# Kernel optimization log

Measured on AMD Instinct MI355X. Metric: run time of the kernel, lower is better.

Reference implementation:

```python
import jax, jax.numpy as jnp
import numpy as np

B, NPG, DEG = 16, 2048, 16          # graphs, nodes per graph, avg degree
N_TOT = B * NPG
E_TOT = N_TOT * DEG
NEG_SLOPE = 0.2


def _gat(x, src, dst, n, w, a_src, a_dst, b):
    # PyG GATConv: concat heads, add self loops, leaky_relu(0.2), segment softmax over targets
    H, C = a_src.shape
    h = (x @ w.T).reshape(n, H, C)                       # [n,H,C]
    sl = jnp.arange(n, dtype=src.dtype)
    s = jnp.concatenate([src, sl])
    d = jnp.concatenate([dst, sl])
    e = jax.nn.leaky_relu((h * a_src).sum(-1)[s] + (h * a_dst).sum(-1)[d], NEG_SLOPE)  # [E+n,H]
    emax = jax.lax.stop_gradient(jax.ops.segment_max(e, d, num_segments=n))
    ee = jnp.exp(e - emax[d])
    alpha = ee / (jax.ops.segment_sum(ee, d, num_segments=n)[d] + 1e-16)
    out = jax.ops.segment_sum(alpha[:, :, None] * h[s], d, num_segments=n)  # [n,H,C]
    return out.reshape(n, H * C) + b


def _gcn(x, src, dst, mask, n, w, b):
    # PyG GCNConv with self loops + symmetric norm; mask = float edge validity
    h = x @ w.T
    deg = jax.ops.segment_sum(mask, dst, num_segments=n) + 1.0  # +1 for self loop
    dinv = jax.lax.rsqrt(deg)
    coef = dinv[src] * dinv[dst] * mask
    out = jax.ops.segment_sum(coef[:, None] * h[src], dst, num_segments=n) + (dinv * dinv)[:, None] * h
    return out + b


def _sag(x, src, dst, mask, b_graphs, npg, k, w_rel, b_rel, w_root):
    # PyG SAGPooling(ratio=0.5): GraphConv score, per-graph top-k, x[perm]*tanh(score[perm]), filter_adj
    n = b_graphs * npg
    agg = jax.ops.segment_sum(mask[:, None] * x[src], dst, num_segments=n)
    score = (agg @ w_rel.T + b_rel + x @ w_root.T)[:, 0]      # [n]
    _, idx = jax.lax.top_k(score.reshape(b_graphs, npg), k)    # [B,k]
    perm = (jnp.arange(b_graphs, dtype=jnp.int32)[:, None] * npg + idx).reshape(-1)
    x_new = x[perm] * jnp.tanh(score[perm])[:, None]
    new_id = jnp.full((n,), -1, jnp.int32).at[perm].set(jnp.arange(b_graphs * k, dtype=jnp.int32))
    ns, nd = new_id[src], new_id[dst]
    valid = mask * ((ns >= 0) & (nd >= 0)).astype(x.dtype)
    return x_new, jnp.maximum(ns, 0), jnp.maximum(nd, 0), valid


def setup_inputs() -> dict:
    key = jax.random.key(0)
    ks = jax.random.split(key, 32)

    def lin(k, o, i):
        return (jax.random.normal(k, (o, i), jnp.float32) / np.sqrt(i)).astype(jnp.float32)

    x = jax.random.normal(ks[0], (N_TOT, 64), jnp.float32)
    off = jnp.repeat(jnp.arange(B, dtype=jnp.int32) * NPG, NPG * DEG)
    src = off + jax.random.randint(ks[1], (E_TOT,), 0, NPG, jnp.int32)
    dst = off + jax.random.randint(ks[2], (E_TOT,), 0, NPG, jnp.int32)
    edge_index = jnp.stack([src, dst])
    batch = jnp.repeat(jnp.arange(B, dtype=jnp.int32), NPG)

    return {
        'x': x, 'edge_index': edge_index, 'batch': batch,
        'gat1_w': lin(ks[3], 256, 64), 'gat1_asrc': lin(ks[4], 4, 64), 'gat1_adst': lin(ks[5], 4, 64),
        'gat1_b': jnp.zeros((256,), jnp.float32),
        'gat2_w': lin(ks[6], 256, 256), 'gat2_asrc': lin(ks[7], 4, 64), 'gat2_adst': lin(ks[8], 4, 64),
        'gat2_b': jnp.zeros((256,), jnp.float32),
        # pooling GCN1: 256 -> 128
        'gcn1_w': lin(ks[9], 128, 256), 'gcn1_b': jnp.zeros((128,), jnp.float32),
        'sag1_wrel': lin(ks[10], 1, 128), 'sag1_brel': jnp.zeros((1,), jnp.float32), 'sag1_wroot': lin(ks[11], 1, 128),
        # pooling GCN2: 128 -> 128
        'gcn2_w': lin(ks[12], 128, 128), 'gcn2_b': jnp.zeros((128,), jnp.float32),
        'sag2_wrel': lin(ks[13], 1, 128), 'sag2_brel': jnp.zeros((1,), jnp.float32), 'sag2_wroot': lin(ks[14], 1, 128),
        # classifier 128 -> 256 -> 128 -> 10
        'fc1_w': lin(ks[15], 256, 128), 'fc1_b': jnp.zeros((256,), jnp.float32),
        'fc2_w': lin(ks[16], 128, 256), 'fc2_b': jnp.zeros((128,), jnp.float32),
        'out_w': lin(ks[17], 10, 128), 'out_b': jnp.zeros((10,), jnp.float32),
    }


def reference(x, edge_index, batch,
              gat1_w, gat1_asrc, gat1_adst, gat1_b,
              gat2_w, gat2_asrc, gat2_adst, gat2_b,
              gcn1_w, gcn1_b, sag1_wrel, sag1_brel, sag1_wroot,
              gcn2_w, gcn2_b, sag2_wrel, sag2_brel, sag2_wroot,
              fc1_w, fc1_b, fc2_w, fc2_b, out_w, out_b):
    n = x.shape[0]
    src, dst = edge_index[0], edge_index[1]
    ones = jnp.ones(src.shape[0], x.dtype)

    # GAT encoder
    h = jax.nn.relu(_gat(x, src, dst, n, gat1_w, gat1_asrc, gat1_adst, gat1_b))
    h = _gat(h, src, dst, n, gat2_w, gat2_asrc, gat2_adst, gat2_b)  # [n,256]

    # GCN + SAGPool x2
    h = jax.nn.relu(_gcn(h, src, dst, ones, n, gcn1_w, gcn1_b))
    k1 = NPG // 2
    h, s1, d1, m1 = _sag(h, src, dst, ones, B, NPG, k1, sag1_wrel, sag1_brel, sag1_wroot)
    h = jax.nn.relu(_gcn(h, s1, d1, m1, B * k1, gcn2_w, gcn2_b))
    k2 = k1 // 2
    h, s2, d2, m2 = _sag(h, s1, d1, m1, B, k1, k2, sag2_wrel, sag2_brel, sag2_wroot)

    # global mean pool (equal-size graphs -> simple reshape-mean; batch vec implied)
    g = h.reshape(B, k2, -1).mean(axis=1)  # [B,128]

    # classifier MLP
    g = jax.nn.relu(g @ fc1_w.T + fc1_b)
    g = jax.nn.relu(g @ fc2_w.T + fc2_b)
    return g @ out_w.T + out_b  # [B,10]
```

## Files before the change

kernel.cpp:

```cpp
#include <hip/hip_runtime.h>

#define N1 32768
#define EE 524288
#define NB 16
#define DEG 16
#define NPG1 2048
#define KK1 1024
#define N2 16384
#define NPG2 1024
#define KK2 512
#define N3 8192

typedef _Float16 half8_t __attribute__((ext_vector_type(8)));
typedef float floatx16 __attribute__((ext_vector_type(16)));

static __device__ __forceinline__ float leaky(float x){ return fmaxf(x, 0.2f*x); }

__global__ void count_dst(const int* __restrict__ dst, int* __restrict__ cnt, int E){
    int i = blockIdx.x*blockDim.x + threadIdx.x;
    if (i < E) atomicAdd(&cnt[dst[i]], 1);
}

__global__ void remap_count(const int* __restrict__ src, const int* __restrict__ dst,
                            const int* __restrict__ nid, int* __restrict__ ns,
                            int* __restrict__ nd, int* __restrict__ cnt, int E){
    int i = blockIdx.x*blockDim.x + threadIdx.x;
    if (i < E){
        int a = nid[src[i]], b = nid[dst[i]];
        ns[i] = a; nd[i] = b;
        if (a >= 0 && b >= 0) atomicAdd(&cnt[b], 1);
    }
}

__global__ void blocksum_k(const int* __restrict__ cnt, int* __restrict__ bs){
    __shared__ int red[4];
    int tid = threadIdx.x;
    int v = cnt[blockIdx.x*256 + tid];
    #pragma unroll
    for (int off = 32; off; off >>= 1) v += __shfl_xor(v, off);
    if ((tid & 63) == 0) red[tid >> 6] = v;
    __syncthreads();
    if (tid == 0) bs[blockIdx.x] = red[0] + red[1] + red[2] + red[3];
}

__global__ void scan_write_k(const int* __restrict__ cnt, const int* __restrict__ bs,
                             int nb, int2* __restrict__ rpx, int* __restrict__ cur,
                             float* __restrict__ dinv){
    __shared__ int sbs[128];
    __shared__ int wsum[4];
    int tid = threadIdx.x;
    int b = blockIdx.x;
    if (tid < nb) sbs[tid] = bs[tid];
    __syncthreads();
    for (int off = 1; off < nb; off <<= 1){
        int v = 0;
        if (tid < nb && tid >= off) v = sbs[tid - off];
        __syncthreads();
        if (tid < nb) sbs[tid] += v;
        __syncthreads();
    }
    int base = (b == 0) ? 0 : sbs[b-1];
    int i = b*256 + tid;
    int c = cnt[i];
    int lane = tid & 63, wv = tid >> 6;
    int x = c;
    #pragma unroll
    for (int off = 1; off < 64; off <<= 1){ int y = __shfl_up(x, off); if (lane >= off) x += y; }
    if (lane == 63) wsum[wv] = x;
    __syncthreads();
    if (tid == 0){ int run = 0; for (int w2 = 0; w2 < 4; w2++){ int t = wsum[w2]; wsum[w2] = run; run += t; } }
    __syncthreads();
    int excl = x - c + wsum[wv];
    int beg = base + excl;
    rpx[i]  = make_int2(beg, beg + c);
    cur[i]  = beg;
    dinv[i] = rsqrtf((float)c + 1.0f);
}

__global__ void scatter1(const int* __restrict__ src, const int* __restrict__ dst,
                         int* __restrict__ cur, int* __restrict__ esrc, int E){
    int i = blockIdx.x*blockDim.x + threadIdx.x;
    if (i < E){ int p = atomicAdd(&cur[dst[i]], 1); esrc[p] = src[i]; }
}

__global__ void scatter2(const int* __restrict__ ns, const int* __restrict__ nd,
                         int* __restrict__ cur, int* __restrict__ esrc, int E){
    int i = blockIdx.x*blockDim.x + threadIdx.x;
    if (i < E){
        int a = ns[i], b = nd[i];
        if (a >= 0 && b >= 0){ int p = atomicAdd(&cur[b], 1); esrc[p] = a; }
    }
}

__global__ void wsplit4(const float* __restrict__ w0, int n0,
                        const float* __restrict__ w1, int n1,
                        const float* __restrict__ w2, int n2,
                        const float* __restrict__ w3, int n3,
                        _Float16* __restrict__ wh, _Float16* __restrict__ wl){
    int i = blockIdx.x*256 + threadIdx.x;
    int n01 = n0 + n1, n012 = n01 + n2, nt = n012 + n3;
    if (i >= nt) return;
    float v = (i < n0) ? w0[i] : (i < n01) ? w1[i - n0] : (i < n012) ? w2[i - n01] : w3[i - n012];
    _Float16 h = (_Float16)v;
    wh[i] = h; wl[i] = (_Float16)(v - (float)h);
}

#define KS 64
static __device__ __forceinline__ int ldsoff(int row, int k8){
    return row*64 + ((k8 ^ (row & 7)) << 3);
}

__global__ __launch_bounds__(256, 2) void gemm_h2(const float* __restrict__ A,
        const _Float16* __restrict__ WHp, const _Float16* __restrict__ WLp,
        float* __restrict__ C, int n, int K, int M,
        const int* __restrict__ perm, const float* __restrict__ tt){
    __shared__ _Float16 sm[4*128*KS];
    _Float16* sAH = sm;
    _Float16* sAL = sm + 128*KS;
    _Float16* sWH = sm + 2*128*KS;
    _Float16* sWL = sm + 3*128*KS;
    int t = threadIdx.x;
    int lane = t & 63;
    int wid = t >> 6;
    int wr = wid >> 1, wc = wid & 1;
    int row0 = blockIdx.x*128, col0 = blockIdx.y*128;
    int srow = t >> 3;
    int sk8  = t & 7;

    floatx16 acc[2][2];
    #pragma unroll
    for (int i = 0; i < 2; i++)
        #pragma unroll
        for (int j = 0; j < 2; j++)
            #pragma unroll
            for (int q = 0; q < 16; q++) acc[i][j][q] = 0.f;

    for (int kk = 0; kk < K; kk += KS){
        #pragma unroll
        for (int p = 0; p < 4; p++){
            int r = srow + p*32;
            int rr = row0 + r;
            int arow = perm ? perm[rr] : rr;
            float tscale = perm ? tt[rr] : 1.0f;
            const float* ga = A + (size_t)arow*K + kk + sk8*8;
            float4 a0 = *(const float4*)ga;
            float4 a1 = *(const float4*)(ga + 4);
            half8_t ahi, alo;
            float av[8] = {a0.x,a0.y,a0.z,a0.w,a1.x,a1.y,a1.z,a1.w};
            #pragma unroll
            for (int q = 0; q < 8; q++){
                float v = av[q] * tscale;
                _Float16 h = (_Float16)v;
                ahi[q] = h; alo[q] = (_Float16)(v - (float)h);
            }
            size_t wo = (size_t)(col0 + r)*K + kk + sk8*8;
            half8_t whi = *(const half8_t*)(WHp + wo);
            half8_t wlo = *(const half8_t*)(WLp + wo);
            int o = ldsoff(r, sk8);
            *(half8_t*)&sAH[o] = ahi;
            *(half8_t*)&sAL[o] = alo;
            *(half8_t*)&sWH[o] = whi;
            *(half8_t*)&sWL[o] = wlo;
        }
        __syncthreads();
        #pragma unroll
        for (int kc = 0; kc < 4; kc++){
            int k8 = kc*2 + (lane >> 5);
            int ra = wr*64 + (lane & 31);
            int rb = wc*64 + (lane & 31);
            half8_t ah0 = *(const half8_t*)&sAH[ldsoff(ra,      k8)];
            half8_t ah1 = *(const half8_t*)&sAH[ldsoff(ra + 32, k8)];
            half8_t al0 = *(const half8_t*)&sAL[ldsoff(ra,      k8)];
            half8_t al1 = *(const half8_t*)&sAL[ldsoff(ra + 32, k8)];
            half8_t bh0 = *(const half8_t*)&sWH[ldsoff(rb,      k8)];
            half8_t bh1 = *(const half8_t*)&sWH[ldsoff(rb + 32, k8)];
            half8_t bl0 = *(const half8_t*)&sWL[ldsoff(rb,      k8)];
            half8_t bl1 = *(const half8_t*)&sWL[ldsoff(rb + 32, k8)];
            acc[0][0] = __builtin_amdgcn_mfma_f32_32x32x16_f16(ah0, bh0, acc[0][0], 0,0,0);
            acc[0][0] = __builtin_amdgcn_mfma_f32_32x32x16_f16(ah0, bl0, acc[0][0], 0,0,0);
            acc[0][0] = __builtin_amdgcn_mfma_f32_32x32x16_f16(al0, bh0, acc[0][0], 0,0,0);
            acc[0][1] = __builtin_amdgcn_mfma_f32_32x32x16_f16(ah0, bh1, acc[0][1], 0,0,0);
            acc[0][1] = __builtin_amdgcn_mfma_f32_32x32x16_f16(ah0, bl1, acc[0][1], 0,0,0);
            acc[0][1] = __builtin_amdgcn_mfma_f32_32x32x16_f16(al0, bh1, acc[0][1], 0,0,0);
            acc[1][0] = __builtin_amdgcn_mfma_f32_32x32x16_f16(ah1, bh0, acc[1][0], 0,0,0);
            acc[1][0] = __builtin_amdgcn_mfma_f32_32x32x16_f16(ah1, bl0, acc[1][0], 0,0,0);
            acc[1][0] = __builtin_amdgcn_mfma_f32_32x32x16_f16(al1, bh0, acc[1][0], 0,0,0);
            acc[1][1] = __builtin_amdgcn_mfma_f32_32x32x16_f16(ah1, bh1, acc[1][1], 0,0,0);
            acc[1][1] = __builtin_amdgcn_mfma_f32_32x32x16_f16(ah1, bl1, acc[1][1], 0,0,0);
            acc[1][1] = __builtin_amdgcn_mfma_f32_32x32x16_f16(al1, bh1, acc[1][1], 0,0,0);
        }
        __syncthreads();
    }
    #pragma unroll
    for (int rt = 0; rt < 2; rt++)
        #pragma unroll
        for (int ct = 0; ct < 2; ct++){
            int baser = row0 + wr*64 + rt*32 + 4*(lane >> 5);
            int c = col0 + wc*64 + ct*32 + (lane & 31);
            #pragma unroll
            for (int r = 0; r < 16; r++){
                int rr = baser + (r & 3) + 8*(r >> 2);
                C[(size_t)rr*M + c] = acc[rt][ct][r];
            }
        }
}

__global__ void attn_pre(const float* __restrict__ h, const float* __restrict__ wsrc,
                         const float* __restrict__ wdst, float* __restrict__ as_,
                         float* __restrict__ ad_){
    int lane = threadIdx.x & 63;
    int w = threadIdx.x >> 6;
    int d = blockIdx.x*4 + w;
    float4 hv = *(const float4*)(h + (size_t)d*256 + lane*4);
    float4 ws = *(const float4*)(wsrc + lane*4);
    float4 wd = *(const float4*)(wdst + lane*4);
    float ps = hv.x*ws.x + hv.y*ws.y + hv.z*ws.z + hv.w*ws.w;
    float pd = hv.x*wd.x + hv.y*wd.y + hv.z*wd.z + hv.w*wd.w;
    #pragma unroll
    for (int m = 8; m; m >>= 1){ ps += __shfl_xor(ps, m); pd += __shfl_xor(pd, m); }
    if ((lane & 15) == 0){
        as_[d*4 + (lane >> 4)] = ps;
        ad_[d*4 + (lane >> 4)] = pd;
    }
}

template<int RELU>
__global__ void gat_agg(const float* __restrict__ h, const float* __restrict__ as_,
                        const float* __restrict__ ad_, const float* __restrict__ bias,
                        const int2* __restrict__ rpx, const int* __restrict__ esrc,
                        float* __restrict__ out){
    int lane = threadIdx.x & 63;
    int nb = gridDim.x;
    int b = blockIdx.x;
    int sb = (b & 7)*(nb >> 3) + (b >> 3);
    int d = __builtin_amdgcn_readfirstlane(sb*4 + (int)(threadIdx.x >> 6));
    int2 re = rpx[d];
    int beg = re.x, end = re.y;

    int hh = lane >> 4;
    float adh = ad_[(d<<2) + hh];
    float aself = as_[(d<<2) + hh];

    float dn[4];
    dn[0] = __expf(leaky(aself + adh)); dn[1] = 0.f; dn[2] = 0.f; dn[3] = 0.f;
    float4 hd = ((const float4*)(h + ((size_t)d<<8)))[lane];
    float4 AX[4];
    AX[0].x = dn[0]*hd.x; AX[0].y = dn[0]*hd.y; AX[0].z = dn[0]*hd.z; AX[0].w = dn[0]*hd.w;
    AX[1] = {0,0,0,0}; AX[2] = {0,0,0,0}; AX[3] = {0,0,0,0};

    int i = beg;
    int endu = beg + ((end - beg) & ~7);
    for (; i < endu; i += 8){
        int s_[8];
        #pragma unroll
        for (int j = 0; j < 8; j++) s_[j] = __builtin_amdgcn_readfirstlane(esrc[i + j]);
        float a_[8];
        #pragma unroll
        for (int j = 0; j < 8; j++) a_[j] = as_[(s_[j]<<2) + hh];
        float4 hv_[8];
        #pragma unroll
        for (int j = 0; j < 8; j++) hv_[j] = ((const float4*)(h + ((size_t)s_[j]<<8)))[lane];
        #pragma unroll
        for (int j = 0; j < 8; j++){
            float x = a_[j] + adh;
            float p = __expf(fmaxf(x, 0.2f*x));
            dn[j & 3] += p;
            AX[j & 3].x = fmaf(p, hv_[j].x, AX[j & 3].x);
            AX[j & 3].y = fmaf(p, hv_[j].y, AX[j & 3].y);
            AX[j & 3].z = fmaf(p, hv_[j].z, AX[j & 3].z);
            AX[j & 3].w = fmaf(p, hv_[j].w, AX[j & 3].w);
        }
    }
    for (; i < end; ++i){
        int s = __builtin_amdgcn_readfirstlane(esrc[i]);
        float x = as_[(s<<2) + hh] + adh;
        float4 hv = ((const float4*)(h + ((size_t)s<<8)))[lane];
        float p = __expf(fmaxf(x, 0.2f*x));
        dn[0] += p;
        AX[0].x = fmaf(p, hv.x, AX[0].x); AX[0].y = fmaf(p, hv.y, AX[0].y);
        AX[0].z = fmaf(p, hv.z, AX[0].z); AX[0].w = fmaf(p, hv.w, AX[0].w);
    }
    float den = ((dn[0] + dn[1]) + (dn[2] + dn[3])) + 1e-16f;
    float r = 1.0f / den;
    int c0 = lane*4;
    float4 bv = *(const float4*)(bias + c0);
    float4 acc;
    acc.x = ((AX[0].x+AX[1].x)+(AX[2].x+AX[3].x))*r + bv.x;
    acc.y = ((AX[0].y+AX[1].y)+(AX[2].y+AX[3].y))*r + bv.y;
    acc.z = ((AX[0].z+AX[1].z)+(AX[2].z+AX[3].z))*r + bv.z;
    acc.w = ((AX[0].w+AX[1].w)+(AX[2].w+AX[3].w))*r + bv.w;
    if (RELU){
        acc.x = fmaxf(acc.x, 0.f); acc.y = fmaxf(acc.y, 0.f);
        acc.z = fmaxf(acc.z, 0.f); acc.w = fmaxf(acc.w, 0.f);
    }
    ((float4*)(out + ((size_t)d<<8)))[lane] = acc;
}

__global__ void gcn_agg_sag(const float* __restrict__ h, const float* __restrict__ dinv,
                            const float* __restrict__ bias,
                            const float* __restrict__ wrel, const float* __restrict__ wroot,
                            const float* __restrict__ brel,
                            const int2* __restrict__ rpx, const int* __restrict__ esrc,
                            float* __restrict__ out, float* __restrict__ Y, float* __restrict__ Z){
    int lane = threadIdx.x & 63;
    int nb = gridDim.x;
    int b = blockIdx.x;
    int sb = (b & 7)*(nb >> 3) + (b >> 3);
    int d = __builtin_amdgcn_readfirstlane(sb*4 + (int)(threadIdx.x >> 6));
    int2 re = rpx[d];
    int beg = re.x, end = re.y;
    float dv = dinv[d];
    int c0 = lane*2;
    float2 hd = ((const float2*)(h + ((size_t)d<<7)))[lane];
    float self = dv*dv;
    float ax[4] = {self*hd.x, 0.f, 0.f, 0.f};
    float ay[4] = {self*hd.y, 0.f, 0.f, 0.f};
    int i = beg;
    int endu = beg + ((end - beg) & ~7);
    for (; i < endu; i += 8){
        int s_[8];
        #pragma unroll
        for (int j = 0; j < 8; j++) s_[j] = __builtin_amdgcn_readfirstlane(esrc[i + j]);
        float di_[8];
        #pragma unroll
        for (int j = 0; j < 8; j++) di_[j] = dinv[s_[j]];
        float2 hv_[8];
        #pragma unroll
        for (int j = 0; j < 8; j++) hv_[j] = ((const float2*)(h + ((size_t)s_[j]<<7)))[lane];
        #pragma unroll
        for (int j = 0; j < 8; j++){
            float coef = di_[j]*dv;
            ax[j & 3] = fmaf(coef, hv_[j].x, ax[j & 3]);
            ay[j & 3] = fmaf(coef, hv_[j].y, ay[j & 3]);
        }
    }
    for (; i < end; ++i){
        int s = __builtin_amdgcn_readfirstlane(esrc[i]);
        float coef = dinv[s]*dv;
        float2 hv = ((const float2*)(h + ((size_t)s<<7)))[lane];
        ax[0] = fmaf(coef, hv.x, ax[0]); ay[0] = fmaf(coef, hv.y, ay[0]);
    }
    float axs = ((ax[0]+ax[1])+(ax[2]+ax[3]));
    float ays = ((ay[0]+ay[1])+(ay[2]+ay[3]));
    axs = fmaxf(axs + bias[c0], 0.f);
    ays = fmaxf(ays + bias[c0+1], 0.f);
    float2 o; o.x = axs; o.y = ays;
    ((float2*)(out + ((size_t)d<<7)))[lane] = o;
    float py = axs*wrel[c0]  + ays*wrel[c0+1];
    float pz = axs*wroot[c0] + ays*wroot[c0+1];
    #pragma unroll
    for (int off = 32; off; off >>= 1){ py += __shfl_xor(py, off); pz += __shfl_xor(pz, off); }
    if (lane == 0){ Y[d] = py; Z[d] = pz + brel[0]; }
}

__global__ __launch_bounds__(1024) void topk_sag(const float* __restrict__ Y,
        const float* __restrict__ Z, const int2* __restrict__ rpx,
        const int* __restrict__ esrc, int npg, int k, int* __restrict__ perm,
        float* __restrict__ ssort, int* __restrict__ nid, int writeNid){
    __shared__ float sc[2048];
    __shared__ unsigned keys[2048];
    __shared__ int hist[256];
    __shared__ int cge[256];
    __shared__ int warpsum[16];
    __shared__ int s_bin, s_need;
    int g = blockIdx.x, tid = threadIdx.x;
    for (int n = tid; n < npg; n += 1024){
        int node = g*npg + n;
        int2 re = rpx[node];
        float s = 0.f;
        int i = re.x;
        for (; i + 3 < re.y; i += 4)
            s += ((Y[esrc[i]] + Y[esrc[i+1]]) + (Y[esrc[i+2]] + Y[esrc[i+3]]));
        for (; i < re.y; ++i) s += Y[esrc[i]];
        float v = s + Z[node];
        sc[n] = v;
        unsigned u = __float_as_uint(v);
        keys[n] = (u & 0x80000000u) ? ~u : (u | 0x80000000u);
    }
    if (tid == 0) s_need = k;
    __syncthreads();
    unsigned prefix = 0u, pmask = 0u;
    #pragma unroll
    for (int shift = 24; shift >= 0; shift -= 8){
        if (tid < 256) hist[tid] = 0;
        __syncthreads();
        for (int i = tid; i < npg; i += 1024){
            unsigned u = keys[i];
            if ((u & pmask) == prefix) atomicAdd(&hist[(u >> shift) & 255u], 1);
        }
        __syncthreads();
        if (tid < 256) cge[tid] = hist[tid];
        __syncthreads();
        for (int off = 1; off < 256; off <<= 1){
            int v = 0;
            if (tid < 256 - off) v = cge[tid + off];
            __syncthreads();
            if (tid < 256) cge[tid] += v;
            __syncthreads();
        }
        int need = s_need;
        if (tid < 256){
            int above = (tid == 255) ? 0 : cge[tid + 1];
            if (cge[tid] >= need && above < need) s_bin = tid;
        }
        __syncthreads();
        if (tid == 0) s_need = need - ((s_bin == 255) ? 0 : cge[s_bin + 1]);
        __syncthreads();
        prefix |= ((unsigned)s_bin) << shift;
        pmask  |= (255u << shift);
        __syncthreads();
    }
    unsigned thr = prefix;
    int m = s_need;
    int i0 = 2*tid, i1 = 2*tid + 1;
    int f0 = 0, f1 = 0;
    if (i0 < npg){
        unsigned u = keys[i0];
        if (u > thr) f0 = 1;
        else if (u == thr){
            int r = 0;
            for (int j = 0; j < i0; j++) r += (keys[j] == thr);
            f0 = (r < m) ? 1 : 0;
        }
    }
    if (i1 < npg){
        unsigned u = keys[i1];
        if (u > thr) f1 = 1;
        else if (u == thr){
            int r = 0;
            for (int j = 0; j < i1; j++) r += (keys[j] == thr);
            f1 = (r < m) ? 1 : 0;
        }
    }
    int pair = f0 + f1;
    int lane = tid & 63, wv = tid >> 6;
    int x = pair;
    #pragma unroll
    for (int off = 1; off < 64; off <<= 1){ int y = __shfl_up(x, off); if (lane >= off) x += y; }
    if (lane == 63) warpsum[wv] = x;
    __syncthreads();
    if (tid == 0){ int run = 0; for (int w2 = 0; w2 < 16; w2++){ int t = warpsum[w2]; warpsum[w2] = run; run += t; } }
    __syncthreads();
    int excl = x - pair + warpsum[wv];
    if (f0){
        int pos = excl;
        int node = g*npg + i0;
        perm[g*k + pos] = node;
        ssort[g*k + pos] = tanhf(sc[i0]);
        if (writeNid) nid[node] = g*k + pos;
    }
    if (f1){
        int pos = excl + f0;
        int node = g*npg + i1;
        perm[g*k + pos] = node;
        ssort[g*k + pos] = tanhf(sc[i1]);
        if (writeNid) nid[node] = g*k + pos;
    }
}

__global__ void pool_mean2(const float* __restrict__ x, const int* __restrict__ perm,
                           const float* __restrict__ ssort, float* __restrict__ g){
    __shared__ float tt[KK2];
    __shared__ float part[128];
    int b = blockIdx.x, t = threadIdx.x;
    tt[t]       = ssort[b*KK2 + t];
    tt[t + 256] = ssort[b*KK2 + t + 256];
    __syncthreads();
    int c = t & 127, half = t >> 7;
    float s = 0.f;
    #pragma unroll 4
    for (int i = half*256; i < half*256 + 256; i++){
        int o = perm[b*KK2 + i];
        s = fmaf(tt[i], x[(size_t)o*128 + c], s);
    }
    if (half) part[c] = s;
    __syncthreads();
    if (!half) g[b*128 + c] = (s + part[c]) * (1.0f/KK2);
}

__global__ void mlp_k(const float* __restrict__ g,
                      const float* __restrict__ fc1w, const float* __restrict__ fc1b,
                      const float* __restrict__ fc2w, const float* __restrict__ fc2b,
                      const float* __restrict__ ow,  const float* __restrict__ ob,
                      float* __restrict__ out){
    __shared__ float gv[128], t1[256], t2[128];
    int b = blockIdx.x, t = threadIdx.x;
    if (t < 128) gv[t] = g[b*128 + t];
    __syncthreads();
    {
        float s = fc1b[t];
        for (int c = 0; c < 128; c++) s += gv[c]*fc1w[t*128 + c];
        t1[t] = fmaxf(s, 0.f);
    }
    __syncthreads();
    if (t < 128){
        float s = fc2b[t];
        for (int c = 0; c < 256; c++) s += t1[c]*fc2w[t*256 + c];
        t2[t] = fmaxf(s, 0.f);
    }
    __syncthreads();
    if (t < 10){
        float s = ob[t];
        for (int c = 0; c < 128; c++) s += t2[c]*ow[t*128 + c];
        out[b*10 + t] = s;
    }
}

extern "C" void kernel_launch(void* const* d_in, const int* in_sizes, int n_in,
                              void* d_out, int out_size, void* d_ws, size_t ws_size,
                              hipStream_t stream){
    (void)in_sizes; (void)n_in; (void)out_size; (void)ws_size;
    const float* x    = (const float*)d_in[0];
    const int*   eidx = (const int*)d_in[1];
    const int*   src  = eidx;
    const int*   dst  = eidx + EE;
    const float* g1w  = (const float*)d_in[3];
    const float* g1as = (const float*)d_in[4];
    const float* g1ad = (const float*)d_in[5];
    const float* g1b  = (const float*)d_in[6];
    const float* g2w  = (const float*)d_in[7];
    const float* g2as = (const float*)d_in[8];
    const float* g2ad = (const float*)d_in[9];
    const float* g2b  = (const float*)d_in[10];
    const float* c1w  = (const float*)d_in[11];
    const float* c1b  = (const float*)d_in[12];
    const float* s1wrel  = (const float*)d_in[13];
    const float* s1brel  = (const float*)d_in[14];
    const float* s1wroot = (const float*)d_in[15];
    const float* c2w  = (const float*)d_in[16];
    const float* c2b  = (const float*)d_in[17];
    const float* s2wrel  = (const float*)d_in[18];
    const float* s2brel  = (const float*)d_in[19];
    const float* s2wroot = (const float*)d_in[20];
    const float* f1w  = (const float*)d_in[21];
    const float* f1b  = (const float*)d_in[22];
    const float* f2w  = (const float*)d_in[23];
    const float* f2b  = (const float*)d_in[24];
    const float* ow   = (const float*)d_in[25];
    const float* ob   = (const float*)d_in[26];
    float* out = (float*)d_out;

    char* ws = (char*)d_ws;
    size_t off = 0;
    auto alloc = [&](size_t bytes)->char*{
        char* p = ws + off;
        off += (bytes + 255) & ~(size_t)255;
        return p;
    };
    float* F0     = (float*)alloc((size_t)N1*256*4);
    float* F1     = (float*)alloc((size_t)N1*256*4);
    float* F2     = (float*)alloc((size_t)N2*128*4);
    float* AS     = (float*)alloc((size_t)N1*4*4);
    float* AD     = (float*)alloc((size_t)N1*4*4);
    int2*  RPX    = (int2*) alloc((size_t)N1*8);
    int*   CUR    = (int*)  alloc((size_t)N1*4);
    int*   EL     = (int*)  alloc((size_t)EE*4);
    float* DINV   = (float*)alloc((size_t)N1*4);
    float* Y      = (float*)alloc((size_t)N1*4);
    float* Z      = (float*)alloc((size_t)N1*4);
    int*   PERM1  = (int*)  alloc((size_t)N2*4);
    float* SSORT1 = (float*)alloc((size_t)N2*4);
    int*   NID    = (int*)  alloc((size_t)N1*4);
    int*   E1S    = (int*)  alloc((size_t)EE*4);
    int*   E1D    = (int*)  alloc((size_t)EE*4);
    int2*  RPX2   = (int2*) alloc((size_t)N2*8);
    int*   CUR2   = (int*)  alloc((size_t)N2*4);
    int*   EL2    = (int*)  alloc((size_t)EE*4);
    float* DINV2  = (float*)alloc((size_t)N2*4);
    int*   PERM2  = (int*)  alloc((size_t)N3*4);
    float* SSORT2 = (float*)alloc((size_t)N3*4);
    float* GBUF   = (float*)alloc((size_t)NB*128*4);
    int*   BS     = (int*)  alloc((size_t)128*4);
    _Float16* WH  = (_Float16*)alloc((size_t)131072*2);
    _Float16* WL  = (_Float16*)alloc((size_t)131072*2);
    const int o_g1 = 0, o_g2 = 16384, o_c1 = 81920, o_c2 = 114688;

    hipMemsetAsync(CUR, 0, (size_t)N1*4, stream);
    count_dst<<<EE/256, 256, 0, stream>>>(dst, CUR, EE);
    blocksum_k<<<N1/256, 256, 0, stream>>>(CUR, BS);
    scan_write_k<<<N1/256, 256, 0, stream>>>(CUR, BS, N1/256, RPX, CUR, DINV);
    scatter1<<<EE/256, 256, 0, stream>>>(src, dst, CUR, EL, EE);
    wsplit4<<<512, 256, 0, stream>>>(g1w, 16384, g2w, 65536, c1w, 32768, c2w, 16384, WH, WL);

    gemm_h2<<<dim3(N1/128, 2), 256, 0, stream>>>(x, WH + o_g1, WL + o_g1, F0, N1, 64, 256, nullptr, nullptr);
    attn_pre<<<N1/4, 256, 0, stream>>>(F0, g1as, g1ad, AS, AD);
    gat_agg<1><<<N1/4, 256, 0, stream>>>(F0, AS, AD, g1b, RPX, EL, F1);

    gemm_h2<<<dim3(N1/128, 2), 256, 0, stream>>>(F1, WH + o_g2, WL + o_g2, F0, N1, 256, 256, nullptr, nullptr);
    attn_pre<<<N1/4, 256, 0, stream>>>(F0, g2as, g2ad, AS, AD);
    gat_agg<0><<<N1/4, 256, 0, stream>>>(F0, AS, AD, g2b, RPX, EL, F1);

    gemm_h2<<<dim3(N1/128, 1), 256, 0, stream>>>(F1, WH + o_c1, WL + o_c1, F0, N1, 256, 128, nullptr, nullptr);
    gcn_agg_sag<<<N1/4, 256, 0, stream>>>(F0, DINV, c1b, s1wrel, s1wroot, s1brel,
                                          RPX, EL, F1, Y, Z);

    hipMemsetAsync(NID, 0xFF, (size_t)N1*4, stream);
    topk_sag<<<NB, 1024, 0, stream>>>(Y, Z, RPX, EL, NPG1, KK1, PERM1, SSORT1, NID, 1);

    hipMemsetAsync(CUR2, 0, (size_t)N2*4, stream);
    remap_count<<<EE/256, 256, 0, stream>>>(src, dst, NID, E1S, E1D, CUR2, EE);
    blocksum_k<<<N2/256, 256, 0, stream>>>(CUR2, BS);
    scan_write_k<<<N2/256, 256, 0, stream>>>(CUR2, BS, N2/256, RPX2, CUR2, DINV2);
    scatter2<<<EE/256, 256, 0, stream>>>(E1S, E1D, CUR2, EL2, EE);

    gemm_h2<<<dim3(N2/128, 1), 256, 0, stream>>>(F1, WH + o_c2, WL + o_c2, F0, N2, 128, 128, PERM1, SSORT1);
    gcn_agg_sag<<<N2/4, 256, 0, stream>>>(F0, DINV2, c2b, s2wrel, s2wroot, s2brel,
                                          RPX2, EL2, F2, Y, Z);

    topk_sag<<<NB, 1024, 0, stream>>>(Y, Z, RPX2, EL2, NPG2, KK2, PERM2, SSORT2, nullptr, 0);

    pool_mean2<<<NB, 256, 0, stream>>>(F2, PERM2, SSORT2, GBUF);
    mlp_k<<<NB, 256, 0, stream>>>(GBUF, f1w, f1b, f2w, f2b, ow, ob, out);
}
```

Baseline: 358.2 us.

## Split SAG scoring into grid-wide kernel and use single-wave radix top-k

Neighbour aggregation for the SAG score moves out of the 16-block top-k kernel into a separate kernel that spreads nodes across the whole grid, one wave per node. Top-k selection is rewritten to run in one 64-lane wave per graph, using shuffles and ballots instead of block-wide syncs and an O(n) tie-rank scan. The NID memset is replaced by writing -1 inside the kernel. This adds an extra launch and a score buffer, and the top-k step now runs on only 16 waves.

```diff
diff --git a/kernel.cpp b/kernel.cpp
--- a/kernel.cpp
+++ b/kernel.cpp
@@ -353,108 +353,93 @@
     if (lane == 0){ Y[d] = py; Z[d] = pz + brel[0]; }
 }
 
-__global__ __launch_bounds__(1024) void topk_sag(const float* __restrict__ Y,
-        const float* __restrict__ Z, const int2* __restrict__ rpx,
-        const int* __restrict__ esrc, int npg, int k, int* __restrict__ perm,
-        float* __restrict__ ssort, int* __restrict__ nid, int writeNid){
-    __shared__ float sc[2048];
+__global__ void sag_lite(const float* __restrict__ Y, const float* __restrict__ Z,
+                         const int2* __restrict__ rpx, const int* __restrict__ esrc,
+                         float* __restrict__ score){
+    int lane = threadIdx.x & 63;
+    int w = threadIdx.x >> 6;
+    int nb = gridDim.x;
+    int b = blockIdx.x;
+    int sb = (b & 7)*(nb >> 3) + (b >> 3);
+    int d = sb*4 + w;
+    int2 re = rpx[d];
+    float s = 0.f;
+    for (int i = re.x + lane; i < re.y; i += 64) s += Y[esrc[i]];
+    #pragma unroll
+    for (int off = 32; off; off >>= 1) s += __shfl_xor(s, off);
+    if (lane == 0) score[d] = s + Z[d];
+}
+
+__global__ __launch_bounds__(64) void topk_wave(const float* __restrict__ score,
+        int npg, int k, int* __restrict__ perm, float* __restrict__ ssort,
+        int* __restrict__ nid, int writeNid){
     __shared__ unsigned keys[2048];
     __shared__ int hist[256];
-    __shared__ int cge[256];
-    __shared__ int warpsum[16];
-    __shared__ int s_bin, s_need;
-    int g = blockIdx.x, tid = threadIdx.x;
-    for (int n = tid; n < npg; n += 1024){
-        int node = g*npg + n;
-        int2 re = rpx[node];
-        float s = 0.f;
-        int i = re.x;
-        for (; i + 3 < re.y; i += 4)
-            s += ((Y[esrc[i]] + Y[esrc[i+1]]) + (Y[esrc[i+2]] + Y[esrc[i+3]]));
-        for (; i < re.y; ++i) s += Y[esrc[i]];
-        float v = s + Z[node];
-        sc[n] = v;
-        unsigned u = __float_as_uint(v);
-        keys[n] = (u & 0x80000000u) ? ~u : (u | 0x80000000u);
-    }
-    if (tid == 0) s_need = k;
-    __syncthreads();
+    int g = blockIdx.x;
+    int lane = threadIdx.x;
+    int nch = npg >> 6;
+    for (int c = 0; c < nch; c++){
+        unsigned u = __float_as_uint(score[g*npg + c*64 + lane]);
+        keys[c*64 + lane] = (u & 0x80000000u) ? ~u : (u | 0x80000000u);
+    }
+    int need = k;
     unsigned prefix = 0u, pmask = 0u;
     #pragma unroll
     for (int shift = 24; shift >= 0; shift -= 8){
-        if (tid < 256) hist[tid] = 0;
-        __syncthreads();
-        for (int i = tid; i < npg; i += 1024){
-            unsigned u = keys[i];
+        #pragma unroll
+        for (int q = 0; q < 4; q++) hist[lane*4 + q] = 0;
+        for (int c = 0; c < nch; c++){
+            unsigned u = keys[c*64 + lane];
             if ((u & pmask) == prefix) atomicAdd(&hist[(u >> shift) & 255u], 1);
         }
-        __syncthreads();
-        if (tid < 256) cge[tid] = hist[tid];
-        __syncthreads();
-        for (int off = 1; off < 256; off <<= 1){
-            int v = 0;
-            if (tid < 256 - off) v = cge[tid + off];
-            __syncthreads();
-            if (tid < 256) cge[tid] += v;
-            __syncthreads();
+        int h0 = hist[lane*4], h1 = hist[lane*4+1], h2 = hist[lane*4+2], h3 = hist[lane*4+3];
+        int s3 = h3, s2 = h2 + s3, s1 = h1 + s2, s0 = h0 + s1;
+        int tot = s0;
+        int suf = tot;
+        #pragma unroll
+        for (int off = 1; off < 64; off <<= 1){
+            int v = __shfl_down(suf, off);
+            if (lane + off < 64) suf += v;
         }
-        int need = s_need;
-        if (tid < 256){
-            int above = (tid == 255) ? 0 : cge[tid + 1];
-            if (cge[tid] >= need && above < need) s_bin = tid;
-        }
-        __syncthreads();
-        if (tid == 0) s_need = need - ((s_bin == 255) ? 0 : cge[s_bin + 1]);
-        __syncthreads();
-        prefix |= ((unsigned)s_bin) << shift;
-        pmask  |= (255u << shift);
-        __syncthreads();
+        int above_quad = suf - tot;
+        int c0 = s0 + above_quad, c1 = s1 + above_quad, c2 = s2 + above_quad, c3 = s3 + above_quad;
+        int sel = -1;
+        if (c0 >= need && c1 < need) sel = 0;
+        if (c1 >= need && c2 < need) sel = 1;
+        if (c2 >= need && c3 < need) sel = 2;
+        if (c3 >= need && above_quad < need) sel = 3;
+        unsigned long long msk = __ballot(sel >= 0);
+        int srcl = __ffsll((long long)msk) - 1;
+        int binq = __shfl(sel, srcl);
+        int bin = srcl*4 + binq;
+        int cge_next = (binq == 0) ? __shfl(c1, srcl) :
+                       (binq == 1) ? __shfl(c2, srcl) :
+                       (binq == 2) ? __shfl(c3, srcl) : __shfl(above_quad, srcl);
+        need -= cge_next;
+        prefix |= ((unsigned)bin) << shift;
+        pmask  |= 255u << shift;
     }
     unsigned thr = prefix;
-    int m = s_need;
-    int i0 = 2*tid, i1 = 2*tid + 1;
-    int f0 = 0, f1 = 0;
-    if (i0 < npg){
-        unsigned u = keys[i0];
-        if (u > thr) f0 = 1;
-        else if (u == thr){
-            int r = 0;
-            for (int j = 0; j < i0; j++) r += (keys[j] == thr);
-            f0 = (r < m) ? 1 : 0;
-        }
-    }
-    if (i1 < npg){
-        unsigned u = keys[i1];
-        if (u > thr) f1 = 1;
-        else if (u == thr){
-            int r = 0;
-            for (int j = 0; j < i1; j++) r += (keys[j] == thr);
-            f1 = (r < m) ? 1 : 0;
-        }
-    }
-    int pair = f0 + f1;
-    int lane = tid & 63, wv = tid >> 6;
-    int x = pair;
-    #pragma unroll
-    for (int off = 1; off < 64; off <<= 1){ int y = __shfl_up(x, off); if (lane >= off) x += y; }
-    if (lane == 63) warpsum[wv] = x;
-    __syncthreads();
-    if (tid == 0){ int run = 0; for (int w2 = 0; w2 < 16; w2++){ int t = warpsum[w2]; warpsum[w2] = run; run += t; } }
-    __syncthreads();
-    int excl = x - pair + warpsum[wv];
-    if (f0){
-        int pos = excl;
-        int node = g*npg + i0;
-        perm[g*k + pos] = node;
-        ssort[g*k + pos] = tanhf(sc[i0]);
-        if (writeNid) nid[node] = g*k + pos;
-    }
-    if (f1){
-        int pos = excl + f0;
-        int node = g*npg + i1;
-        perm[g*k + pos] = node;
-        ssort[g*k + pos] = tanhf(sc[i1]);
-        if (writeNid) nid[node] = g*k + pos;
+    int m = need;
+    unsigned long long below = (lane == 63) ? 0x7FFFFFFFFFFFFFFFull : ((1ull << lane) - 1ull);
+    int base = 0, eqbase = 0;
+    for (int c = 0; c < nch; c++){
+        unsigned u = keys[c*64 + lane];
+        bool gt = u > thr;
+        bool eq = (u == thr);
+        unsigned long long meq = __ballot(eq);
+        int eqrank = eqbase + __popcll(meq & below);
+        bool take = gt || (eq && eqrank < m);
+        unsigned long long mtk = __ballot(take);
+        int pos = base + __popcll(mtk & below);
+        int node = g*npg + c*64 + lane;
+        if (take){
+            perm[g*k + pos] = node;
+            ssort[g*k + pos] = tanhf(score[node]);
+            if (writeNid) nid[node] = g*k + pos;
+        } else if (writeNid) nid[node] = -1;
+        base += __popcll(mtk);
+        eqbase += __popcll(meq);
     }
 }
 
@@ -556,6 +541,7 @@
     int*   CUR    = (int*)  alloc((size_t)N1*4);
     int*   EL     = (int*)  alloc((size_t)EE*4);
     float* DINV   = (float*)alloc((size_t)N1*4);
+    float* SCORE  = (float*)alloc((size_t)N1*4);
     float* Y      = (float*)alloc((size_t)N1*4);
     float* Z      = (float*)alloc((size_t)N1*4);
     int*   PERM1  = (int*)  alloc((size_t)N2*4);
@@ -594,8 +580,8 @@
     gcn_agg_sag<<<N1/4, 256, 0, stream>>>(F0, DINV, c1b, s1wrel, s1wroot, s1brel,
                                           RPX, EL, F1, Y, Z);
 
-    hipMemsetAsync(NID, 0xFF, (size_t)N1*4, stream);
-    topk_sag<<<NB, 1024, 0, stream>>>(Y, Z, RPX, EL, NPG1, KK1, PERM1, SSORT1, NID, 1);
+    sag_lite<<<N1/4, 256, 0, stream>>>(Y, Z, RPX, EL, SCORE);
+    topk_wave<<<NB, 64, 0, stream>>>(SCORE, NPG1, KK1, PERM1, SSORT1, NID, 1);
 
     hipMemsetAsync(CUR2, 0, (size_t)N2*4, stream);
     remap_count<<<EE/256, 256, 0, stream>>>(src, dst, NID, E1S, E1D, CUR2, EE);
@@ -607,7 +593,8 @@
     gcn_agg_sag<<<N2/4, 256, 0, stream>>>(F0, DINV2, c2b, s2wrel, s2wroot, s2brel,
                                           RPX2, EL2, F2, Y, Z);
 
-    topk_sag<<<NB, 1024, 0, stream>>>(Y, Z, RPX2, EL2, NPG2, KK2, PERM2, SSORT2, nullptr, 0);
+    sag_lite<<<N2/4, 256, 0, stream>>>(Y, Z, RPX2, EL2, SCORE);
+    topk_wave<<<NB, 64, 0, stream>>>(SCORE, NPG2, KK2, PERM2, SSORT2, nullptr, 0);
 
     pool_mean2<<<NB, 256, 0, stream>>>(F2, PERM2, SSORT2, GBUF);
     mlp_k<<<NB, 256, 0, stream>>>(GBUF, f1w, f1b, f2w, f2b, ow, ob, out);
```

Result: faster. 335.5 us (-6.3%).
